# Kernel optimization log

Hardware: AMD Instinct MI355X
Metric: run time of the kernel (lower is better)

## Reference

```python
import jax, jax.numpy as jnp
import numpy as np

D_MODEL, D_INNER, D_STATE, D_CONV, DT_RANK = 4, 8, 16, 4, 1


def _build_perms(N, H, W):
    # center-out 2D spatial order
    yy, xx = np.meshgrid(np.arange(H), np.arange(W), indexing='ij')
    cy, cx = H // 2, W // 2
    d2 = (yy - cy) ** 2 + (xx - cx) ** 2
    sp = np.argsort(d2.reshape(-1), kind='stable')          # (H*W,)
    HW = H * W
    # scanA: for each frame t, full center-out spatial sweep
    scanA = (np.arange(N)[:, None] * HW + sp[None, :]).reshape(-1)
    # scanB: for each spatial pos (in center-out order), zig-zag over frames
    fwd = np.arange(N)
    bwd = fwd[::-1]
    tids = np.where((np.arange(HW) % 2 == 0)[:, None], fwd[None, :], bwd[None, :])  # (HW, N)
    scanB = (tids * HW + sp[:, None]).reshape(-1)
    perms = np.stack([scanA, scanB, scanA[::-1], scanB[::-1]], axis=0)  # (4, L)
    return jnp.asarray(perms)


def _dwconv1d(x_bcl, w, b, pad, groups):
    # x: (B, C, L), w: (C, 1, K) depthwise
    y = jax.lax.conv_general_dilated(x_bcl, w, (1,), [pad],
                                     feature_group_count=groups,
                                     dimension_numbers=('NCH', 'OIH', 'NCH'))
    return y + b[None, :, None]


def _forward(x, dwconv_w, dwconv_b, in_proj_w, conv1d_w, conv1d_b,
             x_proj_w, dt_proj_w, dt_proj_b, A_log, Dp, out_proj_w, ln_g, ln_b):
    B, N, H, W = x.shape
    L = N * H * W
    perms = _build_perms(N, H, W)                 # (4, L) int, static
    xf = x.reshape(B, L)
    seqs = xf[:, perms]                            # (B, 4, L) gather along 4 scans
    seqs = _dwconv1d(seqs, dwconv_w, dwconv_b, (1, 1), 4)
    u = jax.nn.silu(seqs.transpose(0, 2, 1))       # (B, L, 4)
    # ---- Mamba(d_model=4) ----
    xz = jnp.einsum('bld,ed->ble', u, in_proj_w)   # (B, L, 2*d_inner)
    xm, z = xz[..., :D_INNER], xz[..., D_INNER:]
    xc = _dwconv1d(xm.transpose(0, 2, 1), conv1d_w, conv1d_b, (D_CONV - 1, 0), D_INNER)
    xm = jax.nn.silu(xc.transpose(0, 2, 1))        # (B, L, 8) causal conv + SiLU
    x_dbl = jnp.einsum('bld,ed->ble', xm, x_proj_w)  # (B, L, dt_rank+2*d_state)
    dt = x_dbl[..., :DT_RANK]
    Bm = x_dbl[..., DT_RANK:DT_RANK + D_STATE]     # (B, L, 16)
    Cm = x_dbl[..., DT_RANK + D_STATE:]            # (B, L, 16)
    dt = jax.nn.softplus(jnp.einsum('blr,dr->bld', dt, dt_proj_w) + dt_proj_b)  # (B, L, 8)
    A = -jnp.exp(A_log)                            # (8, 16)
    dA = jnp.exp(dt[..., None] * A)                # (B, L, 8, 16)
    dBx = dt[..., None] * Bm[:, :, None, :] * xm[..., None]  # (B, L, 8, 16)

    def step(h, inp):
        dA_t, dBx_t, C_t = inp
        h = dA_t * h + dBx_t                       # (B, 8, 16)
        return h, jnp.einsum('bds,bs->bd', h, C_t)

    h0 = jnp.zeros((B, D_INNER, D_STATE), x.dtype)
    _, ys = jax.lax.scan(step, h0, (dA.transpose(1, 0, 2, 3),
                                    dBx.transpose(1, 0, 2, 3),
                                    Cm.transpose(1, 0, 2)))
    y = ys.transpose(1, 0, 2) + xm * Dp            # (B, L, 8)
    y = y * jax.nn.silu(z)
    out = jnp.einsum('bld,ed->ble', y, out_proj_w)  # (B, L, 4)
    # ---- LayerNorm(4) ----
    mu = out.mean(-1, keepdims=True)
    var = ((out - mu) ** 2).mean(-1, keepdims=True)
    out = (out - mu) * jax.lax.rsqrt(var + 1e-5) * ln_g + ln_b
    # rec[:, inv[i]] = out[:, :, i]  <=>  rec_i = out[:, perms[i], i]
    rec = jnp.take_along_axis(out, perms.T[None], axis=1)  # (B, L, 4)
    return rec.mean(-1).reshape(B, N, H, W)


def setup_inputs() -> dict:
    key = jax.random.key(0)
    ks = jax.random.split(key, 12)
    s = 0.1
    x = jax.random.normal(ks[0], (4, 6, 128, 128), jnp.float32)
    return {
        'x': x,
        'dwconv_w': jax.random.normal(ks[1], (4, 1, 3), jnp.float32) * s,
        'dwconv_b': jnp.zeros((4,), jnp.float32),
        'in_proj_w': jax.random.normal(ks[2], (2 * D_INNER, D_MODEL), jnp.float32) * s,
        'conv1d_w': jax.random.normal(ks[3], (D_INNER, 1, D_CONV), jnp.float32) * s,
        'conv1d_b': jnp.zeros((D_INNER,), jnp.float32),
        'x_proj_w': jax.random.normal(ks[4], (DT_RANK + 2 * D_STATE, D_INNER), jnp.float32) * s,
        'dt_proj_w': jax.random.normal(ks[5], (D_INNER, DT_RANK), jnp.float32) * s,
        'dt_proj_b': jnp.full((D_INNER,), -2.0, jnp.float32),
        'A_log': jnp.log(jnp.tile(jnp.arange(1, D_STATE + 1, dtype=jnp.float32), (D_INNER, 1))),
        'Dp': jnp.ones((D_INNER,), jnp.float32),
        'out_proj_w': jax.random.normal(ks[6], (D_MODEL, D_INNER), jnp.float32) * s,
        'ln_g': jnp.ones((4,), jnp.float32),
        'ln_b': jnp.zeros((4,), jnp.float32),
    }


def reference(x, dwconv_w, dwconv_b, in_proj_w, conv1d_w, conv1d_b,
              x_proj_w, dt_proj_w, dt_proj_b, A_log, Dp, out_proj_w, ln_g, ln_b):
    return _forward(x, dwconv_w, dwconv_b, in_proj_w, conv1d_w, conv1d_b,
                    x_proj_w, dt_proj_w, dt_proj_b, A_log, Dp, out_proj_w, ln_g, ln_b)
```

## Files before the change

### kernel.cpp

```cpp
#include <hip/hip_runtime.h>
#include <math.h>

#define HWSZ  16384
#define LTOT  98304
#define NB    4
#define TCH   96
#define NCH   1024
#define GCH   64
#define NGRP  16
#define SD    100

__device__ __forceinline__ float siluf(float x){
  return x * __builtin_amdgcn_rcpf(1.f + __expf(-x));
}
__device__ __forceinline__ float softplusf(float x){
  return fmaxf(x, 0.f) + __logf(1.f + __expf(-fabsf(x)));
}

__device__ __forceinline__ float red16(float x){
  int v;
  v = __float_as_int(x);
  x += __int_as_float(__builtin_amdgcn_update_dpp(0, v, 0xB1, 0xF, 0xF, true));
  v = __float_as_int(x);
  x += __int_as_float(__builtin_amdgcn_update_dpp(0, v, 0x4E, 0xF, 0xF, true));
  v = __float_as_int(x);
  x += __int_as_float(__builtin_amdgcn_update_dpp(0, v, 0x141, 0xF, 0xF, true));
  v = __float_as_int(x);
  x += __int_as_float(__builtin_amdgcn_update_dpp(0, v, 0x140, 0xF, 0xF, true));
  return x;
}

__device__ __forceinline__ int rho0(int i, const int* __restrict__ sp){
  int n = i >> 14; int r = i & (HWSZ - 1);
  return (n << 14) + sp[r];
}
__device__ __forceinline__ int rho1(int i, const int* __restrict__ sp){
  unsigned ui = (unsigned)i;
  unsigned r = ui / 6u; unsigned n = ui - r * 6u;
  unsigned t = (r & 1u) ? (5u - n) : n;
  return (int)((t << 14) + (unsigned)sp[r]);
}

__global__ __launch_bounds__(256) void k_rank(int* __restrict__ sp){
  __shared__ int hist[8193];
  __shared__ int part[256];
  const int tid = threadIdx.x;
  for (int v = tid; v < 8193; v += 256) hist[v] = 0;
  __syncthreads();
  for (int jj = tid; jj < HWSZ; jj += 256){
    int dy = (jj >> 7) - 64, dx = (jj & 127) - 64;
    atomicAdd(&hist[dy*dy + dx*dx], 1);
  }
  __syncthreads();
  const int base = tid * 33;
  {
    int sum = 0;
    for (int m = 0; m < 33; ++m){ int v = base + m; if (v < 8193) sum += hist[v]; }
    part[tid] = sum;
  }
  __syncthreads();
  if (tid == 0){
    int run = 0;
    for (int t = 0; t < 256; ++t){ int c = part[t]; part[t] = run; run += c; }
  }
  __syncthreads();
  {
    int run = part[tid];
    for (int m = 0; m < 33; ++m){
      int v = base + m;
      if (v < 8193){ int c = hist[v]; hist[v] = run; run += c; }
    }
  }
  __syncthreads();

  const int j = blockIdx.x * 256 + tid;
  const int y = j >> 7, x = j & 127;
  const int dy = y - 64, dx = x - 64;
  const int v = dy*dy + dx*dx;
  int cnt = hist[v];
  const int r = __float2int_rd(sqrtf((float)v));
  int yp0 = 64 - r; if (yp0 < 0) yp0 = 0;
  int yp1 = 64 + r + 1; if (yp1 > y) yp1 = y;
  for (int yp = yp0; yp < yp1; ++yp){
    int dyp = yp - 64;
    int tt = v - dyp*dyp;
    int rr = __float2int_rn(sqrtf((float)tt));
    if (rr * rr == tt){
      cnt += (rr <= 64) ? 1 : 0;
      cnt += (rr >= 1 && rr <= 63) ? 1 : 0;
    }
  }
  if (x > 64) cnt += 1;
  sp[cnt] = j;
}

__global__ __launch_bounds__(128, 4)
void k_scan(const float* __restrict__ X,
            const float* __restrict__ dww, const float* __restrict__ dwb,
            const float* __restrict__ ipw,
            const float* __restrict__ c1w, const float* __restrict__ c1b,
            const float* __restrict__ xpw,
            const float* __restrict__ dtpw, const float* __restrict__ dtpb,
            const float* __restrict__ Alog,
            const int* __restrict__ sp,
            float* __restrict__ chA, float* __restrict__ chB,
            float* __restrict__ y0g, float4* __restrict__ ug4)
{
  const int c = blockIdx.x, b = blockIdx.y;
  const int c0 = c * TCH;
  const int tid = threadIdx.x;
  const float* Xb = X + (size_t)b * LTOT;

  __shared__ __align__(16) float s_pre[(TCH + 3) * 9];
  __shared__ __align__(16) float s_dt[8 * SD];
  __shared__ __align__(16) float s_dxm[8 * SD];
  __shared__ __align__(16) float s_Bv[16 * SD];
  __shared__ __align__(16) float s_Cv[16 * SD];

  if (tid < TCH + 3){
    const int m = tid;
    const int i = c0 - 3 + m;
    if (i < 0){
      #pragma unroll
      for (int d = 0; d < 8; ++d) s_pre[m*9 + d] = 0.f;
    } else {
      const int i2 = LTOT - 1 - i;
      const bool okm = (i > 0), okp = (i < LTOT - 1);
      int q[12];
      q[0]  = okm ? rho0(i - 1, sp) : 0;
      q[1]  =       rho0(i,     sp);
      q[2]  = okp ? rho0(i + 1, sp) : 0;
      q[3]  = okm ? rho1(i - 1, sp) : 0;
      q[4]  =       rho1(i,     sp);
      q[5]  = okp ? rho1(i + 1, sp) : 0;
      q[6]  = okm ? rho0(i2 + 1, sp) : 0;
      q[7]  =       rho0(i2,     sp);
      q[8]  = okp ? rho0(i2 - 1, sp) : 0;
      q[9]  = okm ? rho1(i2 + 1, sp) : 0;
      q[10] =       rho1(i2,     sp);
      q[11] = okp ? rho1(i2 - 1, sp) : 0;
      float xv[12];
      #pragma unroll
      for (int t = 0; t < 12; ++t) xv[t] = Xb[q[t]];
      if (!okm){ xv[0] = 0.f; xv[3] = 0.f; xv[6] = 0.f; xv[9]  = 0.f; }
      if (!okp){ xv[2] = 0.f; xv[5] = 0.f; xv[8] = 0.f; xv[11] = 0.f; }
      float u[4];
      #pragma unroll
      for (int k = 0; k < 4; ++k){
        float acc = dwb[k];
        acc = fmaf(dww[k*3+0], xv[k*3+0], acc);
        acc = fmaf(dww[k*3+1], xv[k*3+1], acc);
        acc = fmaf(dww[k*3+2], xv[k*3+2], acc);
        u[k] = siluf(acc);
      }
      ug4[(size_t)b * LTOT + i] = make_float4(u[0], u[1], u[2], u[3]);
      #pragma unroll
      for (int d = 0; d < 8; ++d){
        float acc =      ipw[d*4+0] * u[0];
        acc = fmaf(ipw[d*4+1], u[1], acc);
        acc = fmaf(ipw[d*4+2], u[2], acc);
        acc = fmaf(ipw[d*4+3], u[3], acc);
        s_pre[m*9 + d] = acc;
      }
    }
  }
  __syncthreads();

  if (tid < TCH){
    const int t = tid;
    float xm[8];
    #pragma unroll
    for (int d = 0; d < 8; ++d){
      float acc = c1b[d];
      #pragma unroll
      for (int tau = 0; tau < 4; ++tau)
        acc = fmaf(c1w[d*4+tau], s_pre[(t+tau)*9 + d], acc);
      xm[d] = siluf(acc);
    }
    float dtr = xpw[0] * xm[0];
    #pragma unroll
    for (int d = 1; d < 8; ++d) dtr = fmaf(xpw[d], xm[d], dtr);
    #pragma unroll
    for (int s = 0; s < 16; ++s){
      float acc = xpw[(1+s)*8] * xm[0];
      #pragma unroll
      for (int d = 1; d < 8; ++d) acc = fmaf(xpw[(1+s)*8+d], xm[d], acc);
      s_Bv[s*SD + t] = acc;
      float acc2 = xpw[(17+s)*8] * xm[0];
      #pragma unroll
      for (int d = 1; d < 8; ++d) acc2 = fmaf(xpw[(17+s)*8+d], xm[d], acc2);
      s_Cv[s*SD + t] = acc2;
    }
    #pragma unroll
    for (int d = 0; d < 8; ++d){
      float dtv = softplusf(fmaf(dtpw[d], dtr, dtpb[d]));
      s_dt[d*SD + t]  = dtv;
      s_dxm[d*SD + t] = dtv * xm[d];
    }
  }
  __syncthreads();

  {
    const int d = tid >> 4, s = tid & 15;
    const float Ads = -__expf(Alog[tid]);
    float h = 0.f, sdt = 0.f;
    const float* pdt = s_dt + d*SD;
    const float* pdx = s_dxm + d*SD;
    const float* pB  = s_Bv + s*SD;
    const float* pC  = s_Cv + s*SD;
    float* yb = y0g + ((size_t)b * NCH + c) * 768 + d * 96;
    for (int t0 = 0; t0 < TCH; t0 += 4){
      const float4 dt4 = *reinterpret_cast<const float4*>(pdt + t0);
      const float4 dx4 = *reinterpret_cast<const float4*>(pdx + t0);
      const float4 B4  = *reinterpret_cast<const float4*>(pB + t0);
      const float4 C4  = *reinterpret_cast<const float4*>(pC + t0);
      sdt += dt4.x + dt4.y + dt4.z + dt4.w;
      float y0, y1, y2, y3;
      { float dA = __expf(dt4.x*Ads); h = fmaf(dA, h, dx4.x*B4.x); y0 = h*C4.x; }
      { float dA = __expf(dt4.y*Ads); h = fmaf(dA, h, dx4.y*B4.y); y1 = h*C4.y; }
      { float dA = __expf(dt4.z*Ads); h = fmaf(dA, h, dx4.z*B4.z); y2 = h*C4.z; }
      { float dA = __expf(dt4.w*Ads); h = fmaf(dA, h, dx4.w*B4.w); y3 = h*C4.w; }
      y0 = red16(y0); y1 = red16(y1); y2 = red16(y2); y3 = red16(y3);
      if (s == 0)
        *reinterpret_cast<float4*>(yb + t0) = make_float4(y0, y1, y2, y3);
    }
    const size_t base = ((size_t)b * NCH + c) * 128 + tid;
    chA[base] = __expf(Ads * sdt);
    chB[base] = h;
  }
}

__global__ __launch_bounds__(128) void k_comb1(const float* __restrict__ chA,
                                               const float* __restrict__ chB,
                                               float* __restrict__ hpre,
                                               float* __restrict__ apre,
                                               float* __restrict__ GA,
                                               float* __restrict__ GB){
  const int j = blockIdx.x;
  const int g = j >> 2, b = j & 3;
  const int idx = threadIdx.x;
  const size_t base = ((size_t)b * NCH + (size_t)g * GCH) * 128 + idx;
  float h = 0.f, a = 1.f;
  float A_[8], B_[8];
  #pragma unroll
  for (int m = 0; m < 8; ++m){ A_[m] = chA[base + (size_t)m*128]; B_[m] = chB[base + (size_t)m*128]; }
  for (int cc = 0; cc < GCH; cc += 8){
    float A2[8], B2[8];
    if (cc + 8 < GCH){
      #pragma unroll
      for (int m = 0; m < 8; ++m){ A2[m] = chA[base + (size_t)(cc+8+m)*128]; B2[m] = chB[base + (size_t)(cc+8+m)*128]; }
    } else {
      #pragma unroll
      for (int m = 0; m < 8; ++m){ A2[m] = 0.f; B2[m] = 0.f; }
    }
    #pragma unroll
    for (int m = 0; m < 8; ++m){
      hpre[base + (size_t)(cc+m)*128] = h;
      apre[base + (size_t)(cc+m)*128] = a;
      h = fmaf(A_[m], h, B_[m]);
      a *= A_[m];
    }
    #pragma unroll
    for (int m = 0; m < 8; ++m){ A_[m] = A2[m]; B_[m] = B2[m]; }
  }
  GA[(size_t)(g*4+b)*128 + idx] = a;
  GB[(size_t)(g*4+b)*128 + idx] = h;
}

#define NBL (NB * LTOT)
__global__ __launch_bounds__(128, 4)
void k_corr(const float4* __restrict__ ug4,
            const float* __restrict__ ipw,
            const float* __restrict__ c1w, const float* __restrict__ c1b,
            const float* __restrict__ xpw,
            const float* __restrict__ dtpw, const float* __restrict__ dtpb,
            const float* __restrict__ Alog, const float* __restrict__ Dp,
            const float* __restrict__ opw,
            const float* __restrict__ lng, const float* __restrict__ lnb,
            const float* __restrict__ hpre, const float* __restrict__ apre,
            const float* __restrict__ GA, const float* __restrict__ GB,
            const float* __restrict__ y0g,
            float* __restrict__ outbuf)
{
  const int c = blockIdx.x, b = blockIdx.y;
  const int c0 = c * TCH;
  const int tid = threadIdx.x;
  const size_t cb = (size_t)b * NCH + c;

  __shared__ __align__(16) float s_pre[(TCH + 3) * 9];
  __shared__ __align__(16) float s_sg[8 * 104];
  __shared__ __align__(16) float s_xm[8 * 96];
  __shared__ __align__(16) float s_Ct[96 * 20];
  __shared__ __align__(16) float s_zs[8 * 96];
  __shared__ __align__(16) float s_hA[256];
  float* s_yf = s_pre;

  {
    const int g = c >> 6;
    const float hp = hpre[cb * 128 + tid];
    const float ap = apre[cb * 128 + tid];
    float Hv = 0.f;
    for (int gp = 0; gp < g; ++gp){
      const float ga = GA[(size_t)gp*512 + (size_t)b*128 + tid];
      const float gb = GB[(size_t)gp*512 + (size_t)b*128 + tid];
      Hv = fmaf(ga, Hv, gb);
    }
    s_hA[tid]       = fmaf(ap, Hv, hp);
    s_hA[128 + tid] = -__expf(Alog[tid]);
  }

  if (tid < TCH + 3){
    const int m = tid;
    const int i = c0 - 3 + m;
    if (i < 0){
      #pragma unroll
      for (int d = 0; d < 8; ++d) s_pre[m*9 + d] = 0.f;
    } else {
      const float4 u4 = ug4[(size_t)b * LTOT + i];
      const float u[4] = {u4.x, u4.y, u4.z, u4.w};
      #pragma unroll
      for (int d = 0; d < 8; ++d){
        float acc =      ipw[d*4+0] * u[0];
        acc = fmaf(ipw[d*4+1], u[1], acc);
        acc = fmaf(ipw[d*4+2], u[2], acc);
        acc = fmaf(ipw[d*4+3], u[3], acc);
        s_pre[m*9 + d] = acc;
      }
      if (m >= 3){
        const int t0 = m - 3;
        #pragma unroll
        for (int d = 0; d < 8; ++d){
          float acc =      ipw[(8+d)*4+0] * u[0];
          acc = fmaf(ipw[(8+d)*4+1], u[1], acc);
          acc = fmaf(ipw[(8+d)*4+2], u[2], acc);
          acc = fmaf(ipw[(8+d)*4+3], u[3], acc);
          s_zs[d*96 + t0] = siluf(acc);
        }
      }
    }
  }
  __syncthreads();

  if (tid < TCH){
    const int t = tid;
    float xm[8];
    #pragma unroll
    for (int d = 0; d < 8; ++d){
      float acc = c1b[d];
      #pragma unroll
      for (int tau = 0; tau < 4; ++tau)
        acc = fmaf(c1w[d*4+tau], s_pre[(t+tau)*9 + d], acc);
      float v = siluf(acc);
      xm[d] = v;
      s_xm[d*96 + t] = v;
    }
    float dtr = xpw[0] * xm[0];
    #pragma unroll
    for (int d = 1; d < 8; ++d) dtr = fmaf(xpw[d], xm[d], dtr);
    float* pct = s_Ct + t*20;
    #pragma unroll
    for (int s = 0; s < 16; ++s){
      float acc2 = xpw[(17+s)*8] * xm[0];
      #pragma unroll
      for (int d = 1; d < 8; ++d) acc2 = fmaf(xpw[(17+s)*8+d], xm[d], acc2);
      pct[s] = acc2;
    }
    #pragma unroll
    for (int d = 0; d < 8; ++d)
      s_sg[d*104 + t] = softplusf(fmaf(dtpw[d], dtr, dtpb[d]));
  }
  __syncthreads();

  if (tid < 8){
    float* ps = s_sg + tid*104;
    float run = 0.f;
    for (int t0 = 0; t0 < TCH; t0 += 4){
      const float4 d4 = *reinterpret_cast<const float4*>(ps + t0);
      float r0 = run + d4.x, r1 = r0 + d4.y, r2 = r1 + d4.z, r3 = r2 + d4.w;
      *reinterpret_cast<float4*>(ps + t0) = make_float4(r0, r1, r2, r3);
      run = r3;
    }
  }
  __syncthreads();

  {
    const int d = tid >> 4, tsub = tid & 15;
    float w[16], A16[16];
    #pragma unroll
    for (int s = 0; s < 16; ++s){
      w[s]   = s_hA[d*16 + s];
      A16[s] = s_hA[128 + d*16 + s];
    }
    const float* py0 = y0g + cb * 768 + d * 96;
    for (int t = tsub; t < TCH; t += 16){
      const float sg = s_sg[d*104 + t];
      float acc = py0[t];
      const float* pc = s_Ct + t*20;
      #pragma unroll
      for (int s4 = 0; s4 < 16; s4 += 4){
        const float4 C4 = *reinterpret_cast<const float4*>(pc + s4);
        acc = fmaf(C4.x, __expf(A16[s4+0]*sg) * w[s4+0], acc);
        acc = fmaf(C4.y, __expf(A16[s4+1]*sg) * w[s4+1], acc);
        acc = fmaf(C4.z, __expf(A16[s4+2]*sg) * w[s4+2], acc);
        acc = fmaf(C4.w, __expf(A16[s4+3]*sg) * w[s4+3], acc);
      }
      s_yf[d*96 + t] = acc;
    }
  }
  __syncthreads();

  if (tid < TCH){
    const int t = tid;
    const int i = c0 + t;
    float y[8];
    #pragma unroll
    for (int d = 0; d < 8; ++d)
      y[d] = (s_yf[d*96 + t] + s_xm[d*96 + t] * Dp[d]) * s_zs[d*96 + t];
    float o[4];
    #pragma unroll
    for (int e = 0; e < 4; ++e){
      float acc = opw[e*8] * y[0];
      #pragma unroll
      for (int d = 1; d < 8; ++d) acc = fmaf(opw[e*8+d], y[d], acc);
      o[e] = acc;
    }
    const float mu = 0.25f * (o[0] + o[1] + o[2] + o[3]);
    const float v0 = o[0] - mu, v1 = o[1] - mu, v2 = o[2] - mu, v3 = o[3] - mu;
    const float inv = rsqrtf(0.25f * (v0*v0 + v1*v1 + v2*v2 + v3*v3) + 1e-5f);
    const size_t base = (size_t)b * LTOT + i;
    outbuf[0*NBL + base] = fmaf(v0 * inv, lng[0], lnb[0]);
    outbuf[1*NBL + base] = fmaf(v1 * inv, lng[1], lnb[1]);
    outbuf[2*NBL + base] = fmaf(v2 * inv, lng[2], lnb[2]);
    outbuf[3*NBL + base] = fmaf(v3 * inv, lng[3], lnb[3]);
  }
}

__global__ __launch_bounds__(256) void k_final(const float* __restrict__ outbuf,
                                               const int* __restrict__ sp,
                                               float* __restrict__ out){
  const int l = blockIdx.x * 256 + threadIdx.x;
  const int b = blockIdx.y;
  const int q0 = rho0(l, sp), q1 = rho1(l, sp);
  const int j  = LTOT - 1 - l;
  const int q2 = rho0(j, sp), q3 = rho1(j, sp);
  const size_t pb = (size_t)b * LTOT;
  out[pb + l] = 0.25f * (outbuf[0*NBL + pb + q0] + outbuf[1*NBL + pb + q1] +
                         outbuf[2*NBL + pb + q2] + outbuf[3*NBL + pb + q3]);
}

extern "C" void kernel_launch(void* const* d_in, const int* in_sizes, int n_in,
                              void* d_out, int out_size, void* d_ws, size_t ws_size,
                              hipStream_t stream) {
  const float* X    = (const float*)d_in[0];
  const float* dww  = (const float*)d_in[1];
  const float* dwb  = (const float*)d_in[2];
  const float* ipw  = (const float*)d_in[3];
  const float* c1w  = (const float*)d_in[4];
  const float* c1b  = (const float*)d_in[5];
  const float* xpw  = (const float*)d_in[6];
  const float* dtpw = (const float*)d_in[7];
  const float* dtpb = (const float*)d_in[8];
  const float* Alog = (const float*)d_in[9];
  const float* Dp   = (const float*)d_in[10];
  const float* opw  = (const float*)d_in[11];
  const float* lng  = (const float*)d_in[12];
  const float* lnb  = (const float*)d_in[13];
  float* out = (float*)d_out;

  int* wsI    = (int*)d_ws;
  int* sp     = wsI;
  float* chA  = (float*)(wsI + 16384);
  float* chB  = chA  + 524288;
  float* hpre = chB  + 524288;
  float* apre = hpre + 524288;
  float* GA   = apre + 524288;
  float* GB   = GA + 8192;
  float4* ug4 = (float4*)(GB + 8192);
  float* y0g  = (float*)(ug4) + (size_t)NB * LTOT * 4;
  float* outbuf = y0g + 3145728;

  k_rank<<<64, 256, 0, stream>>>(sp);
  k_scan<<<dim3(NCH, NB), 128, 0, stream>>>(X, dww, dwb, ipw, c1w, c1b, xpw,
      dtpw, dtpb, Alog, sp, chA, chB, y0g, ug4);
  k_comb1<<<64, 128, 0, stream>>>(chA, chB, hpre, apre, GA, GB);
  k_corr<<<dim3(NCH, NB), 128, 0, stream>>>(ug4, ipw, c1w, c1b, xpw,
      dtpw, dtpb, Alog, Dp, opw, lng, lnb, hpre, apre, GA, GB, y0g, outbuf);
  k_final<<<dim3(LTOT / 256, NB), 256, 0, stream>>>(outbuf, sp, out);
}
```

Measured before the change: 184.4 us.

## Fuse all stages into one persistent cooperative kernel with grid syncs

Replaces the five separate kernel launches with one cooperative persistent kernel that loops over tasks per phase and separates phases with grid-wide syncs. The rank computation is rewritten to count lattice points analytically per thread, which removes the shared histogram and prefix sum. The aim is to cut launch overhead and inter-kernel gaps. In exchange, grid syncs add cost, occupancy is capped, and each thread now runs a 128-iteration loop with integer square roots to compute the rank.

```diff
diff --git a/kernel.cpp b/kernel.cpp
--- a/kernel.cpp
+++ b/kernel.cpp
@@ -1,5 +1,8 @@
 #include <hip/hip_runtime.h>
+#include <hip/hip_cooperative_groups.h>
 #include <math.h>
+
+namespace cg = cooperative_groups;
 
 #define HWSZ  16384
 #define LTOT  98304
@@ -9,6 +12,21 @@
 #define GCH   64
 #define NGRP  16
 #define SD    100
+#define NBL   (NB * LTOT)
+#define NTASK (NCH * NB)
+#define FTASK (NBL / 128)
+
+#define O_PRE 0
+#define O_DT  892
+#define O_DXM 1692
+#define O_BV  2492
+#define O_CV  4092
+#define C_SG  892
+#define C_XM  1724
+#define C_CT  2492
+#define C_ZS  4412
+#define C_HA  5180
+#define SMEMF 5692
 
 __device__ __forceinline__ float siluf(float x){
   return x * __builtin_amdgcn_rcpf(1.f + __expf(-x));
@@ -30,6 +48,13 @@
   return x;
 }
 
+__device__ __forceinline__ int isqrt_floor(int v){
+  int r = __float2int_rn(sqrtf((float)v));
+  if (r * r > v) --r;
+  else if ((r + 1) * (r + 1) <= v) ++r;
+  return r;
+}
+
 __device__ __forceinline__ int rho0(int i, const int* __restrict__ sp){
   int n = i >> 14; int r = i & (HWSZ - 1);
   return (n << 14) + sp[r];
@@ -41,432 +66,390 @@
   return (int)((t << 14) + (unsigned)sp[r]);
 }
 
-__global__ __launch_bounds__(256) void k_rank(int* __restrict__ sp){
-  __shared__ int hist[8193];
-  __shared__ int part[256];
+struct Params {
+  const float* X;
+  const float* dww; const float* dwb;
+  const float* ipw;
+  const float* c1w; const float* c1b;
+  const float* xpw;
+  const float* dtpw; const float* dtpb;
+  const float* Alog; const float* Dp;
+  const float* opw;
+  const float* lng; const float* lnb;
+  int* sp;
+  float* chA; float* chB; float* hpre; float* apre;
+  float* GA; float* GB;
+  float4* ug4; float* y0g; float* outbuf; float* out;
+};
+
+__global__ __launch_bounds__(128, 4)
+void k_mega(Params p)
+{
+  __shared__ __align__(16) float smem[SMEMF];
+  cg::grid_group grid = cg::this_grid();
   const int tid = threadIdx.x;
-  for (int v = tid; v < 8193; v += 256) hist[v] = 0;
-  __syncthreads();
-  for (int jj = tid; jj < HWSZ; jj += 256){
-    int dy = (jj >> 7) - 64, dx = (jj & 127) - 64;
-    atomicAdd(&hist[dy*dy + dx*dx], 1);
+  const int nbk = gridDim.x;
+
+  for (int task = blockIdx.x; task < HWSZ / 128; task += nbk){
+    const int j = task * 128 + tid;
+    const int y = j >> 7, x = j & 127;
+    const int dy = y - 64, dx = x - 64;
+    const int v = dy*dy + dx*dx;
+    int cnt = 0;
+    for (int yy = 0; yy < 128; ++yy){
+      int dyy = yy - 64;
+      int w = v - dyy*dyy;
+      if (w > 0){
+        int m = isqrt_floor(w - 1);
+        int lo = m < 64 ? m : 64;
+        int hi = m < 63 ? m : 63;
+        cnt += lo + hi + 1;
+      }
+    }
+    {
+      const int r = isqrt_floor(v);
+      int yp0 = 64 - r; if (yp0 < 0) yp0 = 0;
+      int yp1 = 64 + r + 1; if (yp1 > y) yp1 = y;
+      for (int yp = yp0; yp < yp1; ++yp){
+        int dyp = yp - 64;
+        int tt = v - dyp*dyp;
+        int rr = isqrt_floor(tt);
+        if (rr * rr == tt){
+          cnt += (rr <= 64) ? 1 : 0;
+          cnt += (rr >= 1 && rr <= 63) ? 1 : 0;
+        }
+      }
+      if (x > 64) cnt += 1;
+    }
+    p.sp[cnt] = j;
   }
-  __syncthreads();
-  const int base = tid * 33;
-  {
-    int sum = 0;
-    for (int m = 0; m < 33; ++m){ int v = base + m; if (v < 8193) sum += hist[v]; }
-    part[tid] = sum;
+  grid.sync();
+
+  for (int task = blockIdx.x; task < NTASK; task += nbk){
+    const int c = task & (NCH - 1), b = task >> 10;
+    const int c0 = c * TCH;
+    const float* Xb = p.X + (size_t)b * LTOT;
+    float* s_pre = smem + O_PRE;
+    float* s_dt  = smem + O_DT;
+    float* s_dxm = smem + O_DXM;
+    float* s_Bv  = smem + O_BV;
+    float* s_Cv  = smem + O_CV;
+
+    if (tid < TCH + 3){
+      const int m = tid;
+      const int i = c0 - 3 + m;
+      if (i < 0){
+        #pragma unroll
+        for (int d = 0; d < 8; ++d) s_pre[m*9 + d] = 0.f;
+      } else {
+        const int i2 = LTOT - 1 - i;
+        const bool okm = (i > 0), okp = (i < LTOT - 1);
+        int q[12];
+        q[0]  = okm ? rho0(i - 1, p.sp) : 0;
+        q[1]  =       rho0(i,     p.sp);
+        q[2]  = okp ? rho0(i + 1, p.sp) : 0;
+        q[3]  = okm ? rho1(i - 1, p.sp) : 0;
+        q[4]  =       rho1(i,     p.sp);
+        q[5]  = okp ? rho1(i + 1, p.sp) : 0;
+        q[6]  = okm ? rho0(i2 + 1, p.sp) : 0;
+        q[7]  =       rho0(i2,     p.sp);
+        q[8]  = okp ? rho0(i2 - 1, p.sp) : 0;
+        q[9]  = okm ? rho1(i2 + 1, p.sp) : 0;
+        q[10] =       rho1(i2,     p.sp);
+        q[11] = okp ? rho1(i2 - 1, p.sp) : 0;
+        float xv[12];
+        #pragma unroll
+        for (int t = 0; t < 12; ++t) xv[t] = Xb[q[t]];
+        if (!okm){ xv[0] = 0.f; xv[3] = 0.f; xv[6] = 0.f; xv[9]  = 0.f; }
+        if (!okp){ xv[2] = 0.f; xv[5] = 0.f; xv[8] = 0.f; xv[11] = 0.f; }
+        float u[4];
+        #pragma unroll
+        for (int k = 0; k < 4; ++k){
+          float acc = p.dwb[k];
+          acc = fmaf(p.dww[k*3+0], xv[k*3+0], acc);
+          acc = fmaf(p.dww[k*3+1], xv[k*3+1], acc);
+          acc = fmaf(p.dww[k*3+2], xv[k*3+2], acc);
+          u[k] = siluf(acc);
+        }
+        p.ug4[(size_t)b * LTOT + i] = make_float4(u[0], u[1], u[2], u[3]);
+        #pragma unroll
+        for (int d = 0; d < 8; ++d){
+          float acc =      p.ipw[d*4+0] * u[0];
+          acc = fmaf(p.ipw[d*4+1], u[1], acc);
+          acc = fmaf(p.ipw[d*4+2], u[2], acc);
+          acc = fmaf(p.ipw[d*4+3], u[3], acc);
+          s_pre[m*9 + d] = acc;
+        }
+      }
+    }
+    __syncthreads();
+
+    if (tid < TCH){
+      const int t = tid;
+      float xm[8];
+      #pragma unroll
+      for (int d = 0; d < 8; ++d){
+        float acc = p.c1b[d];
+        #pragma unroll
+        for (int tau = 0; tau < 4; ++tau)
+          acc = fmaf(p.c1w[d*4+tau], s_pre[(t+tau)*9 + d], acc);
+        xm[d] = siluf(acc);
+      }
+      float dtr = p.xpw[0] * xm[0];
+      #pragma unroll
+      for (int d = 1; d < 8; ++d) dtr = fmaf(p.xpw[d], xm[d], dtr);
+      #pragma unroll
+      for (int s = 0; s < 16; ++s){
+        float acc = p.xpw[(1+s)*8] * xm[0];
+        #pragma unroll
+        for (int d = 1; d < 8; ++d) acc = fmaf(p.xpw[(1+s)*8+d], xm[d], acc);
+        s_Bv[s*SD + t] = acc;
+        float acc2 = p.xpw[(17+s)*8] * xm[0];
+        #pragma unroll
+        for (int d = 1; d < 8; ++d) acc2 = fmaf(p.xpw[(17+s)*8+d], xm[d], acc2);
+        s_Cv[s*SD + t] = acc2;
+      }
+      #pragma unroll
+      for (int d = 0; d < 8; ++d){
+        float dtv = softplusf(fmaf(p.dtpw[d], dtr, p.dtpb[d]));
+        s_dt[d*SD + t]  = dtv;
+        s_dxm[d*SD + t] = dtv * xm[d];
+      }
+    }
+    __syncthreads();
+
+    {
+      const int d = tid >> 4, s = tid & 15;
+      const float Ads = -__expf(p.Alog[tid]);
+      float h = 0.f, sdt = 0.f;
+      const float* pdt = s_dt + d*SD;
+      const float* pdx = s_dxm + d*SD;
+      const float* pB  = s_Bv + s*SD;
+      const float* pC  = s_Cv + s*SD;
+      float* yb = p.y0g + ((size_t)b * NCH + c) * 768 + d * 96;
+      for (int t0 = 0; t0 < TCH; t0 += 4){
+        const float4 dt4 = *reinterpret_cast<const float4*>(pdt + t0);
+        const float4 dx4 = *reinterpret_cast<const float4*>(pdx + t0);
+        const float4 B4  = *reinterpret_cast<const float4*>(pB + t0);
+        const float4 C4  = *reinterpret_cast<const float4*>(pC + t0);
+        sdt += dt4.x + dt4.y + dt4.z + dt4.w;
+        float y0, y1, y2, y3;
+        { float dA = __expf(dt4.x*Ads); h = fmaf(dA, h, dx4.x*B4.x); y0 = h*C4.x; }
+        { float dA = __expf(dt4.y*Ads); h = fmaf(dA, h, dx4.y*B4.y); y1 = h*C4.y; }
+        { float dA = __expf(dt4.z*Ads); h = fmaf(dA, h, dx4.z*B4.z); y2 = h*C4.z; }
+        { float dA = __expf(dt4.w*Ads); h = fmaf(dA, h, dx4.w*B4.w); y3 = h*C4.w; }
+        y0 = red16(y0); y1 = red16(y1); y2 = red16(y2); y3 = red16(y3);
+        if (s == 0)
+          *reinterpret_cast<float4*>(yb + t0) = make_float4(y0, y1, y2, y3);
+      }
+      const size_t base = ((size_t)b * NCH + c) * 128 + tid;
+      p.chA[base] = __expf(Ads * sdt);
+      p.chB[base] = h;
+    }
+    __syncthreads();
   }
-  __syncthreads();
-  if (tid == 0){
-    int run = 0;
-    for (int t = 0; t < 256; ++t){ int c = part[t]; part[t] = run; run += c; }
+  grid.sync();
+
+  for (int task = blockIdx.x; task < NGRP * NB; task += nbk){
+    const int g = task >> 2, b = task & 3;
+    const size_t base = ((size_t)b * NCH + (size_t)g * GCH) * 128 + tid;
+    float h = 0.f, a = 1.f;
+    float A_[8], B_[8];
+    #pragma unroll
+    for (int m = 0; m < 8; ++m){ A_[m] = p.chA[base + (size_t)m*128]; B_[m] = p.chB[base + (size_t)m*128]; }
+    for (int cc = 0; cc < GCH; cc += 8){
+      float A2[8], B2[8];
+      if (cc + 8 < GCH){
+        #pragma unroll
+        for (int m = 0; m < 8; ++m){ A2[m] = p.chA[base + (size_t)(cc+8+m)*128]; B2[m] = p.chB[base + (size_t)(cc+8+m)*128]; }
+      } else {
+        #pragma unroll
+        for (int m = 0; m < 8; ++m){ A2[m] = 0.f; B2[m] = 0.f; }
+      }
+      #pragma unroll
+      for (int m = 0; m < 8; ++m){
+        p.hpre[base + (size_t)(cc+m)*128] = h;
+        p.apre[base + (size_t)(cc+m)*128] = a;
+        h = fmaf(A_[m], h, B_[m]);
+        a *= A_[m];
+      }
+      #pragma unroll
+      for (int m = 0; m < 8; ++m){ A_[m] = A2[m]; B_[m] = B2[m]; }
+    }
+    p.GA[(size_t)(g*4+b)*128 + tid] = a;
+    p.GB[(size_t)(g*4+b)*128 + tid] = h;
   }
-  __syncthreads();
-  {
-    int run = part[tid];
-    for (int m = 0; m < 33; ++m){
-      int v = base + m;
-      if (v < 8193){ int c = hist[v]; hist[v] = run; run += c; }
-    }
+  grid.sync();
+
+  for (int task = blockIdx.x; task < NTASK; task += nbk){
+    const int c = task & (NCH - 1), b = task >> 10;
+    const int c0 = c * TCH;
+    const size_t cb = (size_t)b * NCH + c;
+    float* s_yf = smem + O_PRE;
+    float* s_sg = smem + C_SG;
+    float* s_xm = smem + C_XM;
+    float* s_Ct = smem + C_CT;
+    float* s_zs = smem + C_ZS;
+    float* s_hA = smem + C_HA;
+
+    {
+      const int g = c >> 6;
+      const float hp = p.hpre[cb * 128 + tid];
+      const float ap = p.apre[cb * 128 + tid];
+      float Hv = 0.f;
+      for (int gp = 0; gp < g; ++gp){
+        const float ga = p.GA[(size_t)gp*512 + (size_t)b*128 + tid];
+        const float gb = p.GB[(size_t)gp*512 + (size_t)b*128 + tid];
+        Hv = fmaf(ga, Hv, gb);
+      }
+      s_hA[tid]       = fmaf(ap, Hv, hp);
+      s_hA[128 + tid] = -__expf(p.Alog[tid]);
+    }
+
+    if (tid < TCH + 3){
+      const int m = tid;
+      const int i = c0 - 3 + m;
+      if (i < 0){
+        #pragma unroll
+        for (int d = 0; d < 8; ++d) s_yf[m*9 + d] = 0.f;
+      } else {
+        const float4 u4 = p.ug4[(size_t)b * LTOT + i];
+        const float u[4] = {u4.x, u4.y, u4.z, u4.w};
+        #pragma unroll
+        for (int d = 0; d < 8; ++d){
+          float acc =      p.ipw[d*4+0] * u[0];
+          acc = fmaf(p.ipw[d*4+1], u[1], acc);
+          acc = fmaf(p.ipw[d*4+2], u[2], acc);
+          acc = fmaf(p.ipw[d*4+3], u[3], acc);
+          s_yf[m*9 + d] = acc;
+        }
+        if (m >= 3){
+          const int t0 = m - 3;
+          #pragma unroll
+          for (int d = 0; d < 8; ++d){
+            float acc =      p.ipw[(8+d)*4+0] * u[0];
+            acc = fmaf(p.ipw[(8+d)*4+1], u[1], acc);
+            acc = fmaf(p.ipw[(8+d)*4+2], u[2], acc);
+            acc = fmaf(p.ipw[(8+d)*4+3], u[3], acc);
+            s_zs[d*96 + t0] = siluf(acc);
+          }
+        }
+      }
+    }
+    __syncthreads();
+
+    if (tid < TCH){
+      const int t = tid;
+      float xm[8];
+      #pragma unroll
+      for (int d = 0; d < 8; ++d){
+        float acc = p.c1b[d];
+        #pragma unroll
+        for (int tau = 0; tau < 4; ++tau)
+          acc = fmaf(p.c1w[d*4+tau], s_yf[(t+tau)*9 + d], acc);
+        float v = siluf(acc);
+        xm[d] = v;
+        s_xm[d*96 + t] = v;
+      }
+      float dtr = p.xpw[0] * xm[0];
+      #pragma unroll
+      for (int d = 1; d < 8; ++d) dtr = fmaf(p.xpw[d], xm[d], dtr);
+      float* pct = s_Ct + t*20;
+      #pragma unroll
+      for (int s = 0; s < 16; ++s){
+        float acc2 = p.xpw[(17+s)*8] * xm[0];
+        #pragma unroll
+        for (int d = 1; d < 8; ++d) acc2 = fmaf(p.xpw[(17+s)*8+d], xm[d], acc2);
+        pct[s] = acc2;
+      }
+      #pragma unroll
+      for (int d = 0; d < 8; ++d)
+        s_sg[d*104 + t] = softplusf(fmaf(p.dtpw[d], dtr, p.dtpb[d]));
+    }
+    __syncthreads();
+
+    if (tid < 8){
+      float* ps = s_sg + tid*104;
+      float run = 0.f;
+      for (int t0 = 0; t0 < TCH; t0 += 4){
+        const float4 d4 = *reinterpret_cast<const float4*>(ps + t0);
+        float r0 = run + d4.x, r1 = r0 + d4.y, r2 = r1 + d4.z, r3 = r2 + d4.w;
+        *reinterpret_cast<float4*>(ps + t0) = make_float4(r0, r1, r2, r3);
+        run = r3;
+      }
+    }
+    __syncthreads();
+
+    {
+      const int d = tid >> 4, tsub = tid & 15;
+      float w[16], A16[16];
+      #pragma unroll
+      for (int s = 0; s < 16; ++s){
+        w[s]   = s_hA[d*16 + s];
+        A16[s] = s_hA[128 + d*16 + s];
+      }
+      const float* py0 = p.y0g + cb * 768 + d * 96;
+      for (int t = tsub; t < TCH; t += 16){
+        const float sg = s_sg[d*104 + t];
+        float acc = py0[t];
+        const float* pc = s_Ct + t*20;
+        #pragma unroll
+        for (int s4 = 0; s4 < 16; s4 += 4){
+          const float4 C4 = *reinterpret_cast<const float4*>(pc + s4);
+          acc = fmaf(C4.x, __expf(A16[s4+0]*sg) * w[s4+0], acc);
+          acc = fmaf(C4.y, __expf(A16[s4+1]*sg) * w[s4+1], acc);
+          acc = fmaf(C4.z, __expf(A16[s4+2]*sg) * w[s4+2], acc);
+          acc = fmaf(C4.w, __expf(A16[s4+3]*sg) * w[s4+3], acc);
+        }
+        s_yf[d*96 + t] = acc;
+      }
+    }
+    __syncthreads();
+
+    if (tid < TCH){
+      const int t = tid;
+      const int i = c0 + t;
+      float y[8];
+      #pragma unroll
+      for (int d = 0; d < 8; ++d)
+        y[d] = (s_yf[d*96 + t] + s_xm[d*96 + t] * p.Dp[d]) * s_zs[d*96 + t];
+      float o[4];
+      #pragma unroll
+      for (int e = 0; e < 4; ++e){
+        float acc = p.opw[e*8] * y[0];
+        #pragma unroll
+        for (int d = 1; d < 8; ++d) acc = fmaf(p.opw[e*8+d], y[d], acc);
+        o[e] = acc;
+      }
+      const float mu = 0.25f * (o[0] + o[1] + o[2] + o[3]);
+      const float v0 = o[0] - mu, v1 = o[1] - mu, v2 = o[2] - mu, v3 = o[3] - mu;
+      const float inv = rsqrtf(0.25f * (v0*v0 + v1*v1 + v2*v2 + v3*v3) + 1e-5f);
+      const size_t base = (size_t)b * LTOT + i;
+      p.outbuf[0*NBL + base] = fmaf(v0 * inv, p.lng[0], p.lnb[0]);
+      p.outbuf[1*NBL + base] = fmaf(v1 * inv, p.lng[1], p.lnb[1]);
+      p.outbuf[2*NBL + base] = fmaf(v2 * inv, p.lng[2], p.lnb[2]);
+      p.outbuf[3*NBL + base] = fmaf(v3 * inv, p.lng[3], p.lnb[3]);
+    }
+    __syncthreads();
   }
-  __syncthreads();
-
-  const int j = blockIdx.x * 256 + tid;
-  const int y = j >> 7, x = j & 127;
-  const int dy = y - 64, dx = x - 64;
-  const int v = dy*dy + dx*dx;
-  int cnt = hist[v];
-  const int r = __float2int_rd(sqrtf((float)v));
-  int yp0 = 64 - r; if (yp0 < 0) yp0 = 0;
-  int yp1 = 64 + r + 1; if (yp1 > y) yp1 = y;
-  for (int yp = yp0; yp < yp1; ++yp){
-    int dyp = yp - 64;
-    int tt = v - dyp*dyp;
-    int rr = __float2int_rn(sqrtf((float)tt));
-    if (rr * rr == tt){
-      cnt += (rr <= 64) ? 1 : 0;
-      cnt += (rr >= 1 && rr <= 63) ? 1 : 0;
-    }
+  grid.sync();
+
+  for (int task = blockIdx.x; task < FTASK; task += nbk){
+    const int idx = task * 128 + tid;
+    const int b = idx / LTOT;
+    const int l = idx - b * LTOT;
+    const int q0 = rho0(l, p.sp), q1 = rho1(l, p.sp);
+    const int j  = LTOT - 1 - l;
+    const int q2 = rho0(j, p.sp), q3 = rho1(j, p.sp);
+    const size_t pb = (size_t)b * LTOT;
+    p.out[pb + l] = 0.25f * (p.outbuf[0*NBL + pb + q0] + p.outbuf[1*NBL + pb + q1] +
+                             p.outbuf[2*NBL + pb + q2] + p.outbuf[3*NBL + pb + q3]);
   }
-  if (x > 64) cnt += 1;
-  sp[cnt] = j;
-}
-
-__global__ __launch_bounds__(128, 4)
-void k_scan(const float* __restrict__ X,
-            const float* __restrict__ dww, const float* __restrict__ dwb,
-            const float* __restrict__ ipw,
-            const float* __restrict__ c1w, const float* __restrict__ c1b,
-            const float* __restrict__ xpw,
-            const float* __restrict__ dtpw, const float* __restrict__ dtpb,
-            const float* __restrict__ Alog,
-            const int* __restrict__ sp,
-            float* __restrict__ chA, float* __restrict__ chB,
-            float* __restrict__ y0g, float4* __restrict__ ug4)
-{
-  const int c = blockIdx.x, b = blockIdx.y;
-  const int c0 = c * TCH;
-  const int tid = threadIdx.x;
-  const float* Xb = X + (size_t)b * LTOT;
-
-  __shared__ __align__(16) float s_pre[(TCH + 3) * 9];
-  __shared__ __align__(16) float s_dt[8 * SD];
-  __shared__ __align__(16) float s_dxm[8 * SD];
-  __shared__ __align__(16) float s_Bv[16 * SD];
-  __shared__ __align__(16) float s_Cv[16 * SD];
-
-  if (tid < TCH + 3){
-    const int m = tid;
-    const int i = c0 - 3 + m;
-    if (i < 0){
-      #pragma unroll
-      for (int d = 0; d < 8; ++d) s_pre[m*9 + d] = 0.f;
-    } else {
-      const int i2 = LTOT - 1 - i;
-      const bool okm = (i > 0), okp = (i < LTOT - 1);
-      int q[12];
-      q[0]  = okm ? rho0(i - 1, sp) : 0;
-      q[1]  =       rho0(i,     sp);
-      q[2]  = okp ? rho0(i + 1, sp) : 0;
-      q[3]  = okm ? rho1(i - 1, sp) : 0;
-      q[4]  =       rho1(i,     sp);
-      q[5]  = okp ? rho1(i + 1, sp) : 0;
-      q[6]  = okm ? rho0(i2 + 1, sp) : 0;
-      q[7]  =       rho0(i2,     sp);
-      q[8]  = okp ? rho0(i2 - 1, sp) : 0;
-      q[9]  = okm ? rho1(i2 + 1, sp) : 0;
-      q[10] =       rho1(i2,     sp);
-      q[11] = okp ? rho1(i2 - 1, sp) : 0;
-      float xv[12];
-      #pragma unroll
-      for (int t = 0; t < 12; ++t) xv[t] = Xb[q[t]];
-      if (!okm){ xv[0] = 0.f; xv[3] = 0.f; xv[6] = 0.f; xv[9]  = 0.f; }
-      if (!okp){ xv[2] = 0.f; xv[5] = 0.f; xv[8] = 0.f; xv[11] = 0.f; }
-      float u[4];
-      #pragma unroll
-      for (int k = 0; k < 4; ++k){
-        float acc = dwb[k];
-        acc = fmaf(dww[k*3+0], xv[k*3+0], acc);
-        acc = fmaf(dww[k*3+1], xv[k*3+1], acc);
-        acc = fmaf(dww[k*3+2], xv[k*3+2], acc);
-        u[k] = siluf(acc);
-      }
-      ug4[(size_t)b * LTOT + i] = make_float4(u[0], u[1], u[2], u[3]);
-      #pragma unroll
-      for (int d = 0; d < 8; ++d){
-        float acc =      ipw[d*4+0] * u[0];
-        acc = fmaf(ipw[d*4+1], u[1], acc);
-        acc = fmaf(ipw[d*4+2], u[2], acc);
-        acc = fmaf(ipw[d*4+3], u[3], acc);
-        s_pre[m*9 + d] = acc;
-      }
-    }
-  }
-  __syncthreads();
-
-  if (tid < TCH){
-    const int t = tid;
-    float xm[8];
-    #pragma unroll
-    for (int d = 0; d < 8; ++d){
-      float acc = c1b[d];
-      #pragma unroll
-      for (int tau = 0; tau < 4; ++tau)
-        acc = fmaf(c1w[d*4+tau], s_pre[(t+tau)*9 + d], acc);
-      xm[d] = siluf(acc);
-    }
-    float dtr = xpw[0] * xm[0];
-    #pragma unroll
-    for (int d = 1; d < 8; ++d) dtr = fmaf(xpw[d], xm[d], dtr);
-    #pragma unroll
-    for (int s = 0; s < 16; ++s){
-      float acc = xpw[(1+s)*8] * xm[0];
-      #pragma unroll
-      for (int d = 1; d < 8; ++d) acc = fmaf(xpw[(1+s)*8+d], xm[d], acc);
-      s_Bv[s*SD + t] = acc;
-      float acc2 = xpw[(17+s)*8] * xm[0];
-      #pragma unroll
-      for (int d = 1; d < 8; ++d) acc2 = fmaf(xpw[(17+s)*8+d], xm[d], acc2);
-      s_Cv[s*SD + t] = acc2;
-    }
-    #pragma unroll
-    for (int d = 0; d < 8; ++d){
-      float dtv = softplusf(fmaf(dtpw[d], dtr, dtpb[d]));
-      s_dt[d*SD + t]  = dtv;
-      s_dxm[d*SD + t] = dtv * xm[d];
-    }
-  }
-  __syncthreads();
-
-  {
-    const int d = tid >> 4, s = tid & 15;
-    const float Ads = -__expf(Alog[tid]);
-    float h = 0.f, sdt = 0.f;
-    const float* pdt = s_dt + d*SD;
-    const float* pdx = s_dxm + d*SD;
-    const float* pB  = s_Bv + s*SD;
-    const float* pC  = s_Cv + s*SD;
-    float* yb = y0g + ((size_t)b * NCH + c) * 768 + d * 96;
-    for (int t0 = 0; t0 < TCH; t0 += 4){
-      const float4 dt4 = *reinterpret_cast<const float4*>(pdt + t0);
-      const float4 dx4 = *reinterpret_cast<const float4*>(pdx + t0);
-      const float4 B4  = *reinterpret_cast<const float4*>(pB + t0);
-      const float4 C4  = *reinterpret_cast<const float4*>(pC + t0);
-      sdt += dt4.x + dt4.y + dt4.z + dt4.w;
-      float y0, y1, y2, y3;
-      { float dA = __expf(dt4.x*Ads); h = fmaf(dA, h, dx4.x*B4.x); y0 = h*C4.x; }
-      { float dA = __expf(dt4.y*Ads); h = fmaf(dA, h, dx4.y*B4.y); y1 = h*C4.y; }
-      { float dA = __expf(dt4.z*Ads); h = fmaf(dA, h, dx4.z*B4.z); y2 = h*C4.z; }
-      { float dA = __expf(dt4.w*Ads); h = fmaf(dA, h, dx4.w*B4.w); y3 = h*C4.w; }
-      y0 = red16(y0); y1 = red16(y1); y2 = red16(y2); y3 = red16(y3);
-      if (s == 0)
-        *reinterpret_cast<float4*>(yb + t0) = make_float4(y0, y1, y2, y3);
-    }
-    const size_t base = ((size_t)b * NCH + c) * 128 + tid;
-    chA[base] = __expf(Ads * sdt);
-    chB[base] = h;
-  }
-}
-
-__global__ __launch_bounds__(128) void k_comb1(const float* __restrict__ chA,
-                                               const float* __restrict__ chB,
-                                               float* __restrict__ hpre,
-                                               float* __restrict__ apre,
-                                               float* __restrict__ GA,
-                                               float* __restrict__ GB){
-  const int j = blockIdx.x;
-  const int g = j >> 2, b = j & 3;
-  const int idx = threadIdx.x;
-  const size_t base = ((size_t)b * NCH + (size_t)g * GCH) * 128 + idx;
-  float h = 0.f, a = 1.f;
-  float A_[8], B_[8];
-  #pragma unroll
-  for (int m = 0; m < 8; ++m){ A_[m] = chA[base + (size_t)m*128]; B_[m] = chB[base + (size_t)m*128]; }
-  for (int cc = 0; cc < GCH; cc += 8){
-    float A2[8], B2[8];
-    if (cc + 8 < GCH){
-      #pragma unroll
-      for (int m = 0; m < 8; ++m){ A2[m] = chA[base + (size_t)(cc+8+m)*128]; B2[m] = chB[base + (size_t)(cc+8+m)*128]; }
-    } else {
-      #pragma unroll
-      for (int m = 0; m < 8; ++m){ A2[m] = 0.f; B2[m] = 0.f; }
-    }
-    #pragma unroll
-    for (int m = 0; m < 8; ++m){
-      hpre[base + (size_t)(cc+m)*128] = h;
-      apre[base + (size_t)(cc+m)*128] = a;
-      h = fmaf(A_[m], h, B_[m]);
-      a *= A_[m];
-    }
-    #pragma unroll
-    for (int m = 0; m < 8; ++m){ A_[m] = A2[m]; B_[m] = B2[m]; }
-  }
-  GA[(size_t)(g*4+b)*128 + idx] = a;
-  GB[(size_t)(g*4+b)*128 + idx] = h;
-}
-
-#define NBL (NB * LTOT)
-__global__ __launch_bounds__(128, 4)
-void k_corr(const float4* __restrict__ ug4,
-            const float* __restrict__ ipw,
-            const float* __restrict__ c1w, const float* __restrict__ c1b,
-            const float* __restrict__ xpw,
-            const float* __restrict__ dtpw, const float* __restrict__ dtpb,
-            const float* __restrict__ Alog, const float* __restrict__ Dp,
-            const float* __restrict__ opw,
-            const float* __restrict__ lng, const float* __restrict__ lnb,
-            const float* __restrict__ hpre, const float* __restrict__ apre,
-            const float* __restrict__ GA, const float* __restrict__ GB,
-            const float* __restrict__ y0g,
-            float* __restrict__ outbuf)
-{
-  const int c = blockIdx.x, b = blockIdx.y;
-  const int c0 = c * TCH;
-  const int tid = threadIdx.x;
-  const size_t cb = (size_t)b * NCH + c;
-
-  __shared__ __align__(16) float s_pre[(TCH + 3) * 9];
-  __shared__ __align__(16) float s_sg[8 * 104];
-  __shared__ __align__(16) float s_xm[8 * 96];
-  __shared__ __align__(16) float s_Ct[96 * 20];
-  __shared__ __align__(16) float s_zs[8 * 96];
-  __shared__ __align__(16) float s_hA[256];
-  float* s_yf = s_pre;
-
-  {
-    const int g = c >> 6;
-    const float hp = hpre[cb * 128 + tid];
-    const float ap = apre[cb * 128 + tid];
-    float Hv = 0.f;
-    for (int gp = 0; gp < g; ++gp){
-      const float ga = GA[(size_t)gp*512 + (size_t)b*128 + tid];
-      const float gb = GB[(size_t)gp*512 + (size_t)b*128 + tid];
-      Hv = fmaf(ga, Hv, gb);
-    }
-    s_hA[tid]       = fmaf(ap, Hv, hp);
-    s_hA[128 + tid] = -__expf(Alog[tid]);
-  }
-
-  if (tid < TCH + 3){
-    const int m = tid;
-    const int i = c0 - 3 + m;
-    if (i < 0){
-      #pragma unroll
-      for (int d = 0; d < 8; ++d) s_pre[m*9 + d] = 0.f;
-    } else {
-      const float4 u4 = ug4[(size_t)b * LTOT + i];
-      const float u[4] = {u4.x, u4.y, u4.z, u4.w};
-      #pragma unroll
-      for (int d = 0; d < 8; ++d){
-        float acc =      ipw[d*4+0] * u[0];
-        acc = fmaf(ipw[d*4+1], u[1], acc);
-        acc = fmaf(ipw[d*4+2], u[2], acc);
-        acc = fmaf(ipw[d*4+3], u[3], acc);
-        s_pre[m*9 + d] = acc;
-      }
-      if (m >= 3){
-        const int t0 = m - 3;
-        #pragma unroll
-        for (int d = 0; d < 8; ++d){
-          float acc =      ipw[(8+d)*4+0] * u[0];
-          acc = fmaf(ipw[(8+d)*4+1], u[1], acc);
-          acc = fmaf(ipw[(8+d)*4+2], u[2], acc);
-          acc = fmaf(ipw[(8+d)*4+3], u[3], acc);
-          s_zs[d*96 + t0] = siluf(acc);
-        }
-      }
-    }
-  }
-  __syncthreads();
-
-  if (tid < TCH){
-    const int t = tid;
-    float xm[8];
-    #pragma unroll
-    for (int d = 0; d < 8; ++d){
-      float acc = c1b[d];
-      #pragma unroll
-      for (int tau = 0; tau < 4; ++tau)
-        acc = fmaf(c1w[d*4+tau], s_pre[(t+tau)*9 + d], acc);
-      float v = siluf(acc);
-      xm[d] = v;
-      s_xm[d*96 + t] = v;
-    }
-    float dtr = xpw[0] * xm[0];
-    #pragma unroll
-    for (int d = 1; d < 8; ++d) dtr = fmaf(xpw[d], xm[d], dtr);
-    float* pct = s_Ct + t*20;
-    #pragma unroll
-    for (int s = 0; s < 16; ++s){
-      float acc2 = xpw[(17+s)*8] * xm[0];
-      #pragma unroll
-      for (int d = 1; d < 8; ++d) acc2 = fmaf(xpw[(17+s)*8+d], xm[d], acc2);
-      pct[s] = acc2;
-    }
-    #pragma unroll
-    for (int d = 0; d < 8; ++d)
-      s_sg[d*104 + t] = softplusf(fmaf(dtpw[d], dtr, dtpb[d]));
-  }
-  __syncthreads();
-
-  if (tid < 8){
-    float* ps = s_sg + tid*104;
-    float run = 0.f;
-    for (int t0 = 0; t0 < TCH; t0 += 4){
-      const float4 d4 = *reinterpret_cast<const float4*>(ps + t0);
-      float r0 = run + d4.x, r1 = r0 + d4.y, r2 = r1 + d4.z, r3 = r2 + d4.w;
-      *reinterpret_cast<float4*>(ps + t0) = make_float4(r0, r1, r2, r3);
-      run = r3;
-    }
-  }
-  __syncthreads();
-
-  {
-    const int d = tid >> 4, tsub = tid & 15;
-    float w[16], A16[16];
-    #pragma unroll
-    for (int s = 0; s < 16; ++s){
-      w[s]   = s_hA[d*16 + s];
-      A16[s] = s_hA[128 + d*16 + s];
-    }
-    const float* py0 = y0g + cb * 768 + d * 96;
-    for (int t = tsub; t < TCH; t += 16){
-      const float sg = s_sg[d*104 + t];
-      float acc = py0[t];
-      const float* pc = s_Ct + t*20;
-      #pragma unroll
-      for (int s4 = 0; s4 < 16; s4 += 4){
-        const float4 C4 = *reinterpret_cast<const float4*>(pc + s4);
-        acc = fmaf(C4.x, __expf(A16[s4+0]*sg) * w[s4+0], acc);
-        acc = fmaf(C4.y, __expf(A16[s4+1]*sg) * w[s4+1], acc);
-        acc = fmaf(C4.z, __expf(A16[s4+2]*sg) * w[s4+2], acc);
-        acc = fmaf(C4.w, __expf(A16[s4+3]*sg) * w[s4+3], acc);
-      }
-      s_yf[d*96 + t] = acc;
-    }
-  }
-  __syncthreads();
-
-  if (tid < TCH){
-    const int t = tid;
-    const int i = c0 + t;
-    float y[8];
-    #pragma unroll
-    for (int d = 0; d < 8; ++d)
-      y[d] = (s_yf[d*96 + t] + s_xm[d*96 + t] * Dp[d]) * s_zs[d*96 + t];
-    float o[4];
-    #pragma unroll
-    for (int e = 0; e < 4; ++e){
-      float acc = opw[e*8] * y[0];
-      #pragma unroll
-      for (int d = 1; d < 8; ++d) acc = fmaf(opw[e*8+d], y[d], acc);
-      o[e] = acc;
-    }
-    const float mu = 0.25f * (o[0] + o[1] + o[2] + o[3]);
-    const float v0 = o[0] - mu, v1 = o[1] - mu, v2 = o[2] - mu, v3 = o[3] - mu;
-    const float inv = rsqrtf(0.25f * (v0*v0 + v1*v1 + v2*v2 + v3*v3) + 1e-5f);
-    const size_t base = (size_t)b * LTOT + i;
-    outbuf[0*NBL + base] = fmaf(v0 * inv, lng[0], lnb[0]);
-    outbuf[1*NBL + base] = fmaf(v1 * inv, lng[1], lnb[1]);
-    outbuf[2*NBL + base] = fmaf(v2 * inv, lng[2], lnb[2]);
-    outbuf[3*NBL + base] = fmaf(v3 * inv, lng[3], lnb[3]);
-  }
-}
-
-__global__ __launch_bounds__(256) void k_final(const float* __restrict__ outbuf,
-                                               const int* __restrict__ sp,
-                                               float* __restrict__ out){
-  const int l = blockIdx.x * 256 + threadIdx.x;
-  const int b = blockIdx.y;
-  const int q0 = rho0(l, sp), q1 = rho1(l, sp);
-  const int j  = LTOT - 1 - l;
-  const int q2 = rho0(j, sp), q3 = rho1(j, sp);
-  const size_t pb = (size_t)b * LTOT;
-  out[pb + l] = 0.25f * (outbuf[0*NBL + pb + q0] + outbuf[1*NBL + pb + q1] +
-                         outbuf[2*NBL + pb + q2] + outbuf[3*NBL + pb + q3]);
 }
 
 extern "C" void kernel_launch(void* const* d_in, const int* in_sizes, int n_in,
                               void* d_out, int out_size, void* d_ws, size_t ws_size,
                               hipStream_t stream) {
-  const float* X    = (const float*)d_in[0];
-  const float* dww  = (const float*)d_in[1];
-  const float* dwb  = (const float*)d_in[2];
-  const float* ipw  = (const float*)d_in[3];
-  const float* c1w  = (const float*)d_in[4];
-  const float* c1b  = (const float*)d_in[5];
-  const float* xpw  = (const float*)d_in[6];
-  const float* dtpw = (const float*)d_in[7];
-  const float* dtpb = (const float*)d_in[8];
-  const float* Alog = (const float*)d_in[9];
-  const float* Dp   = (const float*)d_in[10];
-  const float* opw  = (const float*)d_in[11];
-  const float* lng  = (const float*)d_in[12];
-  const float* lnb  = (const float*)d_in[13];
-  float* out = (float*)d_out;
-
   int* wsI    = (int*)d_ws;
   int* sp     = wsI;
   float* chA  = (float*)(wsI + 16384);
@@ -479,11 +462,30 @@
   float* y0g  = (float*)(ug4) + (size_t)NB * LTOT * 4;
   float* outbuf = y0g + 3145728;
 
-  k_rank<<<64, 256, 0, stream>>>(sp);
-  k_scan<<<dim3(NCH, NB), 128, 0, stream>>>(X, dww, dwb, ipw, c1w, c1b, xpw,
-      dtpw, dtpb, Alog, sp, chA, chB, y0g, ug4);
-  k_comb1<<<64, 128, 0, stream>>>(chA, chB, hpre, apre, GA, GB);
-  k_corr<<<dim3(NCH, NB), 128, 0, stream>>>(ug4, ipw, c1w, c1b, xpw,
-      dtpw, dtpb, Alog, Dp, opw, lng, lnb, hpre, apre, GA, GB, y0g, outbuf);
-  k_final<<<dim3(LTOT / 256, NB), 256, 0, stream>>>(outbuf, sp, out);
-}
+  Params prm;
+  prm.X    = (const float*)d_in[0];
+  prm.dww  = (const float*)d_in[1];
+  prm.dwb  = (const float*)d_in[2];
+  prm.ipw  = (const float*)d_in[3];
+  prm.c1w  = (const float*)d_in[4];
+  prm.c1b  = (const float*)d_in[5];
+  prm.xpw  = (const float*)d_in[6];
+  prm.dtpw = (const float*)d_in[7];
+  prm.dtpb = (const float*)d_in[8];
+  prm.Alog = (const float*)d_in[9];
+  prm.Dp   = (const float*)d_in[10];
+  prm.opw  = (const float*)d_in[11];
+  prm.lng  = (const float*)d_in[12];
+  prm.lnb  = (const float*)d_in[13];
+  prm.sp = sp; prm.chA = chA; prm.chB = chB; prm.hpre = hpre; prm.apre = apre;
+  prm.GA = GA; prm.GB = GB; prm.ug4 = ug4; prm.y0g = y0g; prm.outbuf = outbuf;
+  prm.out = (float*)d_out;
+
+  int maxb = 0;
+  if (hipOccupancyMaxActiveBlocksPerMultiprocessor(&maxb, k_mega, 128, 0) != hipSuccess || maxb < 1)
+    maxb = 6;
+  if (maxb > 6) maxb = 6;
+  dim3 grid(256 * maxb), block(128);
+  void* args[] = { (void*)&prm };
+  hipLaunchCooperativeKernel(k_mega, grid, block, args, 0u, stream);
+}
```

Measured after the change: 682.1 us. 270% more time.
